# Kernel tuning notes

Measured on AMD Instinct MI355X. Metric: run time of the kernel, lower is better.

The kernel has to match this reference:

```python
import jax, jax.numpy as jnp
import numpy as np

EPS = 1e-5

def _binarize(t):
    # torch Binarize(det) = sign(); .data trick makes autograd see identity (STE)
    return t + jax.lax.stop_gradient(jnp.sign(t) - t)

def _groupnorm1(h, gamma, beta):
    # GroupNorm(num_groups=1): normalize over all channels per sample. h: [B, C]
    mu = jnp.mean(h, axis=1, keepdims=True)
    var = jnp.mean((h - mu) ** 2, axis=1, keepdims=True)
    return (h - mu) * jax.lax.rsqrt(var + EPS) * gamma + beta

def setup_inputs() -> dict:
    key = jax.random.key(0)
    ks = jax.random.split(key, 10)
    B, F, C = 262144, 126, 2
    x = jax.random.normal(ks[0], (B, 1, 1, F), dtype=jnp.float32)
    conv_w = jax.random.normal(ks[1], (F, 1, 1, F), dtype=jnp.float32) * 0.1  # [out_c,in_c,kh,kw]
    gn1_w = jnp.ones((F,), jnp.float32); gn1_b = jnp.zeros((F,), jnp.float32)
    gn2_w = jnp.ones((F,), jnp.float32); gn2_b = jnp.zeros((F,), jnp.float32)
    lin_w = jax.random.normal(ks[2], (C, F), dtype=jnp.float32) * 0.1
    lin_b = jnp.zeros((C,), jnp.float32)
    gn3_w = jnp.ones((C,), jnp.float32); gn3_b = jnp.zeros((C,), jnp.float32)
    return {"x": x, "conv_w": conv_w, "gn1_w": gn1_w, "gn1_b": gn1_b,
            "gn2_w": gn2_w, "gn2_b": gn2_b, "lin_w": lin_w, "lin_b": lin_b,
            "gn3_w": gn3_w, "gn3_b": gn3_b}

def reference(x, conv_w, gn1_w, gn1_b, gn2_w, gn2_b, lin_w, lin_b, gn3_w, gn3_b):
    B = x.shape[0]
    F = conv_w.shape[0]
    # Conv2d(1,126,(1,126)) on [B,1,1,126] collapses to a GEMM over the width axis
    xb = _binarize(x.reshape(B, F))          # [B,126], values in {-1,0,+1}
    wb = _binarize(conv_w.reshape(F, F))     # [126,126]
    h = jnp.einsum('bf,cf->bc', xb, wb)      # conv output, 1x1 spatial squeezed
    h = _groupnorm1(h, gn1_w, gn1_b)         # GroupNorm(1,126) on [B,126,1,1]
    h = jnp.clip(h, -1.0, 1.0)               # Hardtanh
    # Flatten is identity here; second GroupNorm(1,126) + Hardtanh
    h = _groupnorm1(h, gn2_w, gn2_b)
    h = jnp.clip(h, -1.0, 1.0)
    # BNNLinear: binarize input and weight, bias added un-binarized
    hb = _binarize(h)
    lwb = _binarize(lin_w)
    out = jnp.einsum('bf,cf->bc', hb, lwb) + lin_b  # [B,2]
    out = _groupnorm1(out, gn3_w, gn3_b)     # GroupNorm(1,2)
    return out
```

## Files before the change

### kernel.cpp

```cpp
#include <hip/hip_runtime.h>
#include <stdint.h>
#include <math.h>

#define FDIM 126
#define TPB 256

template <typename F>
__device__ __forceinline__ double pw126d(F a) {
    #pragma clang fp contract(off)
    double r0=a(0), r1=a(1), r2=a(2), r3=a(3), r4=a(4), r5=a(5), r6=a(6), r7=a(7);
    for (int i = 8; i < 120; i += 8) {
        r0 += a(i);   r1 += a(i+1); r2 += a(i+2); r3 += a(i+3);
        r4 += a(i+4); r5 += a(i+5); r6 += a(i+6); r7 += a(i+7);
    }
    double res = ((r0 + r1) + (r2 + r3)) + ((r4 + r5) + (r6 + r7));
    res += a(120); res += a(121); res += a(122); res += a(123); res += a(124); res += a(125);
    return res;
}
template <typename F>
__device__ __forceinline__ float pw126f(F a) {
    #pragma clang fp contract(off)
    float r0=a(0), r1=a(1), r2=a(2), r3=a(3), r4=a(4), r5=a(5), r6=a(6), r7=a(7);
    for (int i = 8; i < 120; i += 8) {
        r0 += a(i);   r1 += a(i+1); r2 += a(i+2); r3 += a(i+3);
        r4 += a(i+4); r5 += a(i+5); r6 += a(i+6); r7 += a(i+7);
    }
    float res = ((r0 + r1) + (r2 + r3)) + ((r4 + r5) + (r6 + r7));
    res += a(120); res += a(121); res += a(122); res += a(123); res += a(124); res += a(125);
    return res;
}

__global__ __launch_bounds__(TPB) void bnn_v14(
    const float* __restrict__ x,
    const float* __restrict__ conv_w,
    const float* __restrict__ gn1_w, const float* __restrict__ gn1_b,
    const float* __restrict__ gn2_w, const float* __restrict__ gn2_b,
    const float* __restrict__ lin_w, const float* __restrict__ lin_b,
    const float* __restrict__ gn3_w, const float* __restrict__ gn3_b,
    float* __restrict__ out, int nrows)
{
    #pragma clang fp contract(off)
    __shared__ ulonglong2 s_ws[FDIM];
    __shared__ ulonglong2 s_wn[FDIM];
    __shared__ float2 s_g1[FDIM];
    __shared__ float2 s_g2[FDIM];
    __shared__ int8_t s_sl0[128];
    __shared__ int8_t s_sl1[128];
    __shared__ int s_flags;
    __shared__ __align__(16) uint8_t s_pool[TPB * 128];

    ulonglong2* s_xs = (ulonglong2*)s_pool;
    ulonglong2* s_xn = (ulonglong2*)(s_pool + 4096);
    uint32_t*   s_h  = (uint32_t*)s_pool;

    const int t = threadIdx.x;
    const int lane = t & 63;
    const int wv = t >> 6;
    const int64_t row0 = (int64_t)blockIdx.x * TPB;
    const int64_t row = row0 + t;
    const bool rowOK = row < (int64_t)nrows;

    if (t == 0) s_flags = 0;
    __syncthreads();

    for (int r = wv; r < FDIM; r += 4) {
        const float* wr = conv_w + (size_t)r * FDIM;
        float v0 = wr[lane];
        float v1 = (lane < FDIM - 64) ? wr[64 + lane] : 0.f;
        uint64_t ss0 = __ballot(v0 < 0.f);
        uint64_t nn0 = __ballot(v0 != 0.f);
        uint64_t ss1 = __ballot(v1 < 0.f);
        uint64_t nn1 = __ballot(v1 != 0.f);
        if (lane == 0) {
            s_ws[r] = make_ulonglong2(ss0, ss1);
            s_wn[r] = make_ulonglong2(nn0, nn1);
            if (__popcll(nn0) + __popcll(nn1) != FDIM) atomicOr(&s_flags, 1);
        }
    }

    #pragma unroll 4
    for (int k = 0; k < 64; ++k) {
        int lr = (wv << 6) + k;
        int64_t r = row0 + lr;
        bool ok = r < (int64_t)nrows;
        const float* xr = x + r * FDIM;
        float v0 = ok ? xr[lane] : 0.f;
        float v1 = (ok && lane < FDIM - 64) ? xr[64 + lane] : 0.f;
        uint64_t ss0 = __ballot(v0 < 0.f);
        uint64_t nn0 = __ballot(v0 != 0.f);
        uint64_t ss1 = __ballot(v1 < 0.f);
        uint64_t nn1 = __ballot(v1 != 0.f);
        if (lane == 0) {
            s_xs[lr] = make_ulonglong2(ss0, ss1);
            s_xn[lr] = make_ulonglong2(nn0, nn1);
        }
    }

    if (t < FDIM) {
        float g1wv = gn1_w[t], g1bv = gn1_b[t];
        float g2wv = gn2_w[t], g2bv = gn2_b[t];
        s_g1[t] = make_float2(g1wv, g1bv);
        s_g2[t] = make_float2(g2wv, g2bv);
        if (g1wv != 1.f || g1bv != 0.f) atomicOr(&s_flags, 2);
        if (g2wv != 1.f || g2bv != 0.f) atomicOr(&s_flags, 4);
        float l0 = lin_w[t], l1 = lin_w[FDIM + t];
        s_sl0[t] = (int8_t)((l0 > 0.f) - (l0 < 0.f));
        s_sl1[t] = (int8_t)((l1 > 0.f) - (l1 < 0.f));
    }
    __syncthreads();
    const int flags = s_flags;

    const ulonglong2 xs = s_xs[t];
    const ulonglong2 xn = s_xn[t];
    const int Kx = __popcll(xn.x) + __popcll(xn.y);
    __syncthreads();

    int sum = 0;
    if (!(flags & 1)) {
        for (int g = 0; g < 32; ++g) {
            uint32_t pack = 0;
            #pragma unroll
            for (int j = 0; j < 4; ++j) {
                int cc = 4 * g + j;
                if (cc < FDIM) {
                    ulonglong2 w = s_ws[cc];
                    int pc = __popcll((xs.x ^ w.x) & xn.x) + __popcll((xs.y ^ w.y) & xn.y);
                    int h = Kx - 2 * pc;
                    sum += h;
                    pack |= (uint32_t)(h & 255) << (8 * j);
                }
            }
            s_h[g * TPB + t] = pack;
        }
    } else {
        for (int g = 0; g < 32; ++g) {
            uint32_t pack = 0;
            #pragma unroll
            for (int j = 0; j < 4; ++j) {
                int cc = 4 * g + j;
                if (cc < FDIM) {
                    ulonglong2 w = s_ws[cc];
                    ulonglong2 wn = s_wn[cc];
                    uint64_t m0 = xn.x & wn.x, m1 = xn.y & wn.y;
                    int pm = __popcll(m0) + __popcll(m1);
                    int pc = __popcll((xs.x ^ w.x) & m0) + __popcll((xs.y ^ w.y) & m1);
                    int h = pm - 2 * pc;
                    sum += h;
                    pack |= (uint32_t)(h & 255) << (8 * j);
                }
            }
            s_h[g * TPB + t] = pack;
        }
    }

    auto hget = [&](int i) -> int {
        return (int)(int8_t)((s_h[(i >> 2) * TPB + t] >> ((i & 3) << 3)) & 255u);
    };

    const float mu1f = (float)sum / 126.0f;
    const float var1f = pw126f([&](int i) -> float {
        #pragma clang fp contract(off)
        float e = (float)hget(i) - mu1f;
        return e * e;
    }) / 126.0f;
    const double r1 = 1.0 / sqrt((double)var1f + 1e-5);

    int ip0 = 0, ip1 = 0;
    if (!(flags & 6)) {
        auto c1f = [&](int i) -> double {
            #pragma clang fp contract(off)
            float e32 = (float)hget(i) - mu1f;
            double y = (double)e32 * r1;
            return fmin(fmax(y, -1.0), 1.0);
        };
        const double mu2 = pw126d(c1f) / 126.0;
        for (int c = 0; c < FDIM; ++c) {
            double z = c1f(c) - mu2;
            int hb = (z > 0.0) - (z < 0.0);
            ip0 += hb * (int)s_sl0[c];
            ip1 += hb * (int)s_sl1[c];
        }
    } else {
        auto c1f = [&](int i) -> double {
            #pragma clang fp contract(off)
            float e32 = (float)hget(i) - mu1f;
            float2 g = s_g1[i];
            double y = (((double)e32 * r1) * (double)g.x) + (double)g.y;
            return fmin(fmax(y, -1.0), 1.0);
        };
        const double mu2 = pw126d(c1f) / 126.0;
        const double var2 = pw126d([&](int i) -> double {
            #pragma clang fp contract(off)
            double e2 = c1f(i) - mu2;
            return e2 * e2;
        }) / 126.0;
        const double r2 = 1.0 / sqrt(var2 + 1e-5);
        for (int c = 0; c < FDIM; ++c) {
            double e2 = c1f(c) - mu2;
            float2 g2 = s_g2[c];
            double z = ((e2 * r2) * (double)g2.x) + (double)g2.y;
            int hb = (z > 0.0) - (z < 0.0);
            ip0 += hb * (int)s_sl0[c];
            ip1 += hb * (int)s_sl1[c];
        }
    }

    if (rowOK) {
        double o0 = (double)ip0 + (double)lin_b[0];
        double o1 = (double)ip1 + (double)lin_b[1];
        double mu = (o0 + o1) / 2.0;
        double d0 = o0 - mu, d1 = o1 - mu;
        double var = ((d0 * d0) + (d1 * d1)) / 2.0;
        double r3 = 1.0 / sqrt(var + 1e-5);
        double q0 = ((d0 * r3) * (double)gn3_w[0]) + (double)gn3_b[0];
        double q1 = ((d1 * r3) * (double)gn3_w[1]) + (double)gn3_b[1];
        reinterpret_cast<float2*>(out)[row] = make_float2((float)q0, (float)q1);
    }
}

extern "C" void kernel_launch(void* const* d_in, const int* in_sizes, int n_in,
                              void* d_out, int out_size, void* d_ws, size_t ws_size,
                              hipStream_t stream) {
    const float* x      = (const float*)d_in[0];
    const float* conv_w = (const float*)d_in[1];
    const float* gn1_w  = (const float*)d_in[2];
    const float* gn1_b  = (const float*)d_in[3];
    const float* gn2_w  = (const float*)d_in[4];
    const float* gn2_b  = (const float*)d_in[5];
    const float* lin_w  = (const float*)d_in[6];
    const float* lin_b  = (const float*)d_in[7];
    const float* gn3_w  = (const float*)d_in[8];
    const float* gn3_b  = (const float*)d_in[9];

    int nrows = in_sizes[0] / FDIM;
    int nblocks = (nrows + TPB - 1) / TPB;
    bnn_v14<<<nblocks, TPB, 0, stream>>>(x, conv_w, gn1_w, gn1_b, gn2_w, gn2_b,
                                         lin_w, lin_b, gn3_w, gn3_b,
                                         (float*)d_out, nrows);
}
```

Baseline: 81.78 us.

## Replace per-element double sign test with integer thresholds via binary search

The first GroupNorm+clamp is monotonic in the integer conv output, so the kernel binary-searches integer thresholds where the normalized value crosses mu2. The final sign loop then compares int8 values against those thresholds instead of evaluating double-precision clamp and subtract for every channel. The variance and mean loops are also rewritten to load each packed dword once and extract its bytes, rather than reloading from shared memory for each element. This cuts double-precision work and LDS traffic per row, at the cost of extra code and relying on monotonicity for exactness.

```diff
diff --git a/kernel.cpp b/kernel.cpp
--- a/kernel.cpp
+++ b/kernel.cpp
@@ -4,6 +4,7 @@
 
 #define FDIM 126
 #define TPB 256
+#define BEXT(u, j) ((int)(int8_t)((u) >> ((j) * 8)))
 
 template <typename F>
 __device__ __forceinline__ double pw126d(F a) {
@@ -17,20 +18,8 @@
     res += a(120); res += a(121); res += a(122); res += a(123); res += a(124); res += a(125);
     return res;
 }
-template <typename F>
-__device__ __forceinline__ float pw126f(F a) {
-    #pragma clang fp contract(off)
-    float r0=a(0), r1=a(1), r2=a(2), r3=a(3), r4=a(4), r5=a(5), r6=a(6), r7=a(7);
-    for (int i = 8; i < 120; i += 8) {
-        r0 += a(i);   r1 += a(i+1); r2 += a(i+2); r3 += a(i+3);
-        r4 += a(i+4); r5 += a(i+5); r6 += a(i+6); r7 += a(i+7);
-    }
-    float res = ((r0 + r1) + (r2 + r3)) + ((r4 + r5) + (r6 + r7));
-    res += a(120); res += a(121); res += a(122); res += a(123); res += a(124); res += a(125);
-    return res;
-}
-
-__global__ __launch_bounds__(TPB) void bnn_v14(
+
+__global__ __launch_bounds__(TPB) void bnn_v15(
     const float* __restrict__ x,
     const float* __restrict__ conv_w,
     const float* __restrict__ gn1_w, const float* __restrict__ gn1_b,
@@ -153,32 +142,110 @@
         }
     }
 
-    auto hget = [&](int i) -> int {
-        return (int)(int8_t)((s_h[(i >> 2) * TPB + t] >> ((i & 3) << 3)) & 255u);
+    auto hdw = [&](int g) -> uint32_t { return s_h[g * TPB + t]; };
+    auto hget = [&](int i) -> int { return BEXT(hdw(i >> 2), i & 3); };
+
+    const float mu1f = (float)sum / 126.0f;
+    float var1f;
+    {
+        uint32_t u0 = hdw(0), u1 = hdw(1);
+        float e;
+        e = (float)BEXT(u0,0) - mu1f; float q0 = e*e;
+        e = (float)BEXT(u0,1) - mu1f; float q1 = e*e;
+        e = (float)BEXT(u0,2) - mu1f; float q2 = e*e;
+        e = (float)BEXT(u0,3) - mu1f; float q3 = e*e;
+        e = (float)BEXT(u1,0) - mu1f; float q4 = e*e;
+        e = (float)BEXT(u1,1) - mu1f; float q5 = e*e;
+        e = (float)BEXT(u1,2) - mu1f; float q6 = e*e;
+        e = (float)BEXT(u1,3) - mu1f; float q7 = e*e;
+        for (int k = 1; k < 15; ++k) {
+            uint32_t a0 = hdw(2*k), a1 = hdw(2*k + 1);
+            e = (float)BEXT(a0,0) - mu1f; q0 += e*e;
+            e = (float)BEXT(a0,1) - mu1f; q1 += e*e;
+            e = (float)BEXT(a0,2) - mu1f; q2 += e*e;
+            e = (float)BEXT(a0,3) - mu1f; q3 += e*e;
+            e = (float)BEXT(a1,0) - mu1f; q4 += e*e;
+            e = (float)BEXT(a1,1) - mu1f; q5 += e*e;
+            e = (float)BEXT(a1,2) - mu1f; q6 += e*e;
+            e = (float)BEXT(a1,3) - mu1f; q7 += e*e;
+        }
+        float res = ((q0 + q1) + (q2 + q3)) + ((q4 + q5) + (q6 + q7));
+        uint32_t u30 = hdw(30), u31 = hdw(31);
+        e = (float)BEXT(u30,0) - mu1f; res += e*e;
+        e = (float)BEXT(u30,1) - mu1f; res += e*e;
+        e = (float)BEXT(u30,2) - mu1f; res += e*e;
+        e = (float)BEXT(u30,3) - mu1f; res += e*e;
+        e = (float)BEXT(u31,0) - mu1f; res += e*e;
+        e = (float)BEXT(u31,1) - mu1f; res += e*e;
+        var1f = res / 126.0f;
+    }
+    const double r1 = 1.0 / sqrt((double)var1f + 1e-5);
+
+    auto c1ofh = [&](int hv) -> double {
+        #pragma clang fp contract(off)
+        float e32 = (float)hv - mu1f;
+        double y = (double)e32 * r1;
+        return fmin(fmax(y, -1.0), 1.0);
     };
-
-    const float mu1f = (float)sum / 126.0f;
-    const float var1f = pw126f([&](int i) -> float {
-        #pragma clang fp contract(off)
-        float e = (float)hget(i) - mu1f;
-        return e * e;
-    }) / 126.0f;
-    const double r1 = 1.0 / sqrt((double)var1f + 1e-5);
 
     int ip0 = 0, ip1 = 0;
     if (!(flags & 6)) {
-        auto c1f = [&](int i) -> double {
-            #pragma clang fp contract(off)
-            float e32 = (float)hget(i) - mu1f;
-            double y = (double)e32 * r1;
-            return fmin(fmax(y, -1.0), 1.0);
-        };
-        const double mu2 = pw126d(c1f) / 126.0;
-        for (int c = 0; c < FDIM; ++c) {
-            double z = c1f(c) - mu2;
-            int hb = (z > 0.0) - (z < 0.0);
-            ip0 += hb * (int)s_sl0[c];
-            ip1 += hb * (int)s_sl1[c];
+        double mu2;
+        {
+            uint32_t u0 = hdw(0), u1 = hdw(1);
+            double q0 = c1ofh(BEXT(u0,0)), q1 = c1ofh(BEXT(u0,1));
+            double q2 = c1ofh(BEXT(u0,2)), q3 = c1ofh(BEXT(u0,3));
+            double q4 = c1ofh(BEXT(u1,0)), q5 = c1ofh(BEXT(u1,1));
+            double q6 = c1ofh(BEXT(u1,2)), q7 = c1ofh(BEXT(u1,3));
+            for (int k = 1; k < 15; ++k) {
+                uint32_t a0 = hdw(2*k), a1 = hdw(2*k + 1);
+                q0 += c1ofh(BEXT(a0,0)); q1 += c1ofh(BEXT(a0,1));
+                q2 += c1ofh(BEXT(a0,2)); q3 += c1ofh(BEXT(a0,3));
+                q4 += c1ofh(BEXT(a1,0)); q5 += c1ofh(BEXT(a1,1));
+                q6 += c1ofh(BEXT(a1,2)); q7 += c1ofh(BEXT(a1,3));
+            }
+            double res = ((q0 + q1) + (q2 + q3)) + ((q4 + q5) + (q6 + q7));
+            uint32_t u30 = hdw(30), u31 = hdw(31);
+            res += c1ofh(BEXT(u30,0)); res += c1ofh(BEXT(u30,1));
+            res += c1ofh(BEXT(u30,2)); res += c1ofh(BEXT(u30,3));
+            res += c1ofh(BEXT(u31,0)); res += c1ofh(BEXT(u31,1));
+            mu2 = res / 126.0;
+        }
+
+        const double c127 = c1ofh(127);
+        int lo1 = -127, hi1 = 127, lo2 = -127, hi2 = 127;
+        #pragma unroll
+        for (int it = 0; it < 8; ++it) {
+            int m1 = (lo1 + hi1) >> 1;
+            bool ge = (c1ofh(m1) >= mu2);
+            hi1 = ge ? m1 : hi1;  lo1 = ge ? lo1 : m1 + 1;
+            int m2 = (lo2 + hi2) >> 1;
+            bool gt = (c1ofh(m2) > mu2);
+            hi2 = gt ? m2 : hi2;  lo2 = gt ? lo2 : m2 + 1;
+        }
+        const int vge = (c127 >= mu2) ? lo1 : 128;
+        const int vgt = (c127 >  mu2) ? lo2 : 128;
+
+        for (int g = 0; g < 31; ++g) {
+            uint32_t u = hdw(g);
+            #pragma unroll
+            for (int j = 0; j < 4; ++j) {
+                int c = 4 * g + j;
+                int hv = BEXT(u, j);
+                int hb = (hv >= vgt) - (hv < vge);
+                ip0 += hb * (int)s_sl0[c];
+                ip1 += hb * (int)s_sl1[c];
+            }
+        }
+        {
+            uint32_t u = hdw(31);
+            #pragma unroll
+            for (int j = 0; j < 2; ++j) {
+                int hv = BEXT(u, j);
+                int hb = (hv >= vgt) - (hv < vge);
+                ip0 += hb * (int)s_sl0[124 + j];
+                ip1 += hb * (int)s_sl1[124 + j];
+            }
         }
     } else {
         auto c1f = [&](int i) -> double {
@@ -234,7 +301,7 @@
 
     int nrows = in_sizes[0] / FDIM;
     int nblocks = (nrows + TPB - 1) / TPB;
-    bnn_v14<<<nblocks, TPB, 0, stream>>>(x, conv_w, gn1_w, gn1_b, gn2_w, gn2_b,
+    bnn_v15<<<nblocks, TPB, 0, stream>>>(x, conv_w, gn1_w, gn1_b, gn2_w, gn2_b,
                                          lin_w, lin_b, gn3_w, gn3_b,
                                          (float*)d_out, nrows);
 }
```

Result: faster. 77.52 us (-5.2%).
